# Kernel optimization log

Measured on AMD Instinct MI355X. Metric: run time of the kernel, lower is better.

The kernel has to match this reference:

```python
import jax, jax.numpy as jnp
import numpy as np

NUM_GRAPHS = 256
BN_EPS = 1e-5


def setup_inputs() -> dict:
    key = jax.random.key(0)
    ks = jax.random.split(key, 16)
    N, E, D_IN, D, L = 100000, 1200000, 4, 64, 3
    inp = {
        "x": jax.random.normal(ks[0], (N, D_IN), dtype=jnp.float32),
        "EdgeID": jax.random.randint(ks[1], (2, E), 0, N, dtype=jnp.int64),
        "EdgeAttr": jax.random.uniform(ks[2], (E,), dtype=jnp.float32),
        "batch": jnp.sort(jax.random.randint(ks[3], (N,), 0, NUM_GRAPHS, dtype=jnp.int64)),
        # embedding Linear(4, 64)
        "W_emb": jax.random.normal(ks[4], (D_IN, D), dtype=jnp.float32) * 0.5,
        "b_emb": jax.random.normal(ks[5], (D,), dtype=jnp.float32) * 0.1,
        # LEConv params stacked over layers: lin1 (bias), lin2 (no bias), lin3 (bias)
        "W1": jax.random.normal(ks[6], (L, D, D), dtype=jnp.float32) * 0.125,
        "b1": jax.random.normal(ks[7], (L, D), dtype=jnp.float32) * 0.1,
        "W2": jax.random.normal(ks[8], (L, D, D), dtype=jnp.float32) * 0.125,
        "W3": jax.random.normal(ks[9], (L, D, D), dtype=jnp.float32) * 0.125,
        "b3": jax.random.normal(ks[10], (L, D), dtype=jnp.float32) * 0.1,
        # BatchNorm affine params per layer
        "gamma": jnp.ones((L, D), dtype=jnp.float32),
        "beta": jnp.zeros((L, D), dtype=jnp.float32),
        # MLP head
        "W_l1": jax.random.normal(ks[11], (D, D), dtype=jnp.float32) * 0.125,
        "b_l1": jax.random.normal(ks[12], (D,), dtype=jnp.float32) * 0.1,
        "W_l2": jax.random.normal(ks[13], (D, 3), dtype=jnp.float32) * 0.125,
        "b_l2": jax.random.normal(ks[14], (3,), dtype=jnp.float32) * 0.1,
    }
    return inp


def reference(x, EdgeID, EdgeAttr, batch, W_emb, b_emb, W1, b1, W2, W3, b3,
              gamma, beta, W_l1, b_l1, W_l2, b_l2):
    N = x.shape[0]
    L = W1.shape[0]
    src, dst = EdgeID[0], EdgeID[1]  # message flows src(j) -> dst(i)

    h = x @ W_emb + b_emb  # [N, 64]; F.dropout(training=False) is a no-op
    for i in range(L):
        a = h @ W1[i] + b1[i]               # lin1(x_j)
        b = h @ W2[i]                       # lin2(x_i)
        msg = EdgeAttr[:, None] * (a[src] - b[dst])  # [E, 64]
        agg = jax.ops.segment_sum(msg, dst, num_segments=N)
        h = agg + h @ W3[i] + b3[i]         # LEConv output
        # BatchNorm (training-mode batch stats over nodes)
        mean = jnp.mean(h, axis=0)
        var = jnp.var(h, axis=0)
        h = gamma[i] * (h - mean) * jax.lax.rsqrt(var + BN_EPS) + beta[i]
        h = jax.nn.relu(h)

    # global mean pool over graphs
    ones = jnp.ones((N,), dtype=h.dtype)
    counts = jax.ops.segment_sum(ones, batch, num_segments=NUM_GRAPHS)
    sums = jax.ops.segment_sum(h, batch, num_segments=NUM_GRAPHS)
    g = sums / jnp.maximum(counts, 1.0)[:, None]  # [G, 64]

    pred = jax.nn.relu(g @ W_l1 + b_l1) @ W_l2 + b_l2  # [G, 3]
    return pred
```

## Files before the change

### kernel.cpp

```cpp
#include <hip/hip_runtime.h>

#define BN_EPS 1e-5f

typedef __attribute__((ext_vector_type(8))) short bf16x8;
typedef __attribute__((ext_vector_type(4))) float f32x4;

__global__ void k_hist(const int* __restrict__ dst, int* __restrict__ deg, int E) {
    int e = blockIdx.x * blockDim.x + threadIdx.x;
    if (e < E) atomicAdd(&deg[dst[e]], 1);
}

__global__ __launch_bounds__(256) void k_blocksum(const int* __restrict__ deg,
                                                  int* __restrict__ bsum, int N) {
    __shared__ int red[256];
    int tid = threadIdx.x;
    int base = blockIdx.x * 1024 + tid * 4;
    int s = 0;
    if (base + 3 < N) {
        int4 v = *(const int4*)&deg[base];
        s = v.x + v.y + v.z + v.w;
    } else {
        for (int i = 0; i < 4; ++i) if (base + i < N) s += deg[base + i];
    }
    red[tid] = s;
    __syncthreads();
    for (int d = 128; d > 0; d >>= 1) {
        if (tid < d) red[tid] += red[tid + d];
        __syncthreads();
    }
    if (tid == 0) bsum[blockIdx.x] = red[0];
}

__global__ __launch_bounds__(1024) void k_scanpartials(int* __restrict__ bsum, int nb) {
    __shared__ int t[1024];
    int tid = threadIdx.x;
    int v = (tid < nb) ? bsum[tid] : 0;
    t[tid] = v;
    __syncthreads();
    for (int d = 1; d < 1024; d <<= 1) {
        int u = (tid >= d) ? t[tid - d] : 0;
        __syncthreads();
        t[tid] += u;
        __syncthreads();
    }
    if (tid < nb) bsum[tid] = t[tid] - v;
}

__global__ __launch_bounds__(256) void k_applyscan(const int* __restrict__ deg,
                                                   const int* __restrict__ bsum,
                                                   int* __restrict__ rowptr,
                                                   int* __restrict__ gcur, int N, int E) {
    __shared__ int red[256];
    int tid = threadIdx.x;
    int base = blockIdx.x * 1024 + tid * 4;
    int v0 = 0, v1 = 0, v2 = 0, v3 = 0;
    if (base + 3 < N) {
        int4 v = *(const int4*)&deg[base];
        v0 = v.x; v1 = v.y; v2 = v.z; v3 = v.w;
    } else {
        if (base < N) v0 = deg[base];
        if (base + 1 < N) v1 = deg[base + 1];
        if (base + 2 < N) v2 = deg[base + 2];
        if (base + 3 < N) v3 = deg[base + 3];
    }
    int s = v0 + v1 + v2 + v3;
    red[tid] = s;
    __syncthreads();
    for (int d = 1; d < 256; d <<= 1) {
        int u = (tid >= d) ? red[tid - d] : 0;
        __syncthreads();
        red[tid] += u;
        __syncthreads();
    }
    int off = bsum[blockIdx.x] + red[tid] - s;
    int r0 = off, r1 = off + v0, r2 = r1 + v1, r3 = r2 + v2;
    if (base < N)     rowptr[base] = r0;
    if (base + 1 < N) rowptr[base + 1] = r1;
    if (base + 2 < N) rowptr[base + 2] = r2;
    if (base + 3 < N) rowptr[base + 3] = r3;
    if ((base & 255) == 0 && base < N) gcur[base >> 8] = r0;
    if (blockIdx.x == 0 && tid == 0) rowptr[N] = E;
}

#define ABLK 8192
__global__ __launch_bounds__(1024) void k_binA(const int* __restrict__ src,
                                               const int* __restrict__ dst,
                                               const float* __restrict__ attr,
                                               int* __restrict__ gcur,
                                               unsigned long long* __restrict__ tmp,
                                               int E, int N) {
    __shared__ int hist[1024];
    __shared__ int lcur[1024];
    int tid = threadIdx.x;
    int NB = (N + 255) >> 8;
    int e0 = blockIdx.x * ABLK;
    int e1 = e0 + ABLK; if (e1 > E) e1 = E;
    for (int i = tid; i < NB; i += 1024) hist[i] = 0;
    __syncthreads();
    for (int e = e0 + tid; e < e1; e += 1024) atomicAdd(&hist[dst[e] >> 8], 1);
    __syncthreads();
    for (int b = tid; b < NB; b += 1024) {
        int hc = hist[b];
        lcur[b] = hc ? atomicAdd(&gcur[b], hc) : 0;
    }
    __syncthreads();
    for (int e = e0 + tid; e < e1; e += 1024) {
        int d = dst[e];
        int pos = atomicAdd(&lcur[d >> 8], 1);
        unsigned long long p = ((unsigned long long)__float_as_uint(attr[e]) << 32) |
                               ((unsigned long long)(d & 255) << 24) |
                               (unsigned int)src[e];
        tmp[pos] = p;
    }
}

__global__ __launch_bounds__(256) void k_binB(const int* __restrict__ rowptr,
                                              const unsigned long long* __restrict__ tmp,
                                              unsigned long long* __restrict__ edata,
                                              int N) {
    __shared__ int cur[256];
    int b = blockIdx.x;
    int tid = threadIdx.x;
    int nb0 = b << 8;
    int node = nb0 + tid;
    cur[tid] = (node < N) ? rowptr[node] : 0;
    int beg = rowptr[nb0];
    int endnode = nb0 + 256; if (endnode > N) endnode = N;
    int end = rowptr[endnode];
    __syncthreads();
    for (int e = beg + tid; e < end; e += 256) {
        unsigned long long p = tmp[e];
        int dl = (int)((p >> 24) & 255);
        int pos = atomicAdd(&cur[dl], 1);
        edata[pos] = (p & 0xFFFFFFFF00000000ull) | ((p & 0xFFFFFFull) << 8);
    }
}

__device__ __forceinline__ void bn_coeff(const float* bs, const float* gam,
                                         const float* bet, int c, float inv_n,
                                         float& sc, float& sh) {
    float mean = bs[c] * inv_n;
    float var = bs[64 + c] * inv_n - mean * mean;
    sc = gam[c] * rsqrtf(fmaxf(var, 0.f) + BN_EPS);
    sh = bet[c] - mean * sc;
}

__global__ void k_gather4(const int* __restrict__ rowptr,
                          const unsigned long long* __restrict__ edata,
                          const float* __restrict__ x,
                          float* __restrict__ g4, float* __restrict__ degw, int N) {
    int n = blockIdx.x * blockDim.x + threadIdx.x;
    if (n >= N) return;
    int beg = rowptr[n], end = rowptr[n + 1];
    float4 a0 = {0.f, 0.f, 0.f, 0.f}, a1 = {0.f, 0.f, 0.f, 0.f};
    float wsum = 0.f;
    int e = beg;
    for (; e + 1 < end; e += 2) {
        unsigned long long p0 = edata[e], p1 = edata[e + 1];
        float w0 = __uint_as_float((unsigned)(p0 >> 32));
        float w1 = __uint_as_float((unsigned)(p1 >> 32));
        float4 v0 = *(const float4*)((const char*)x + (((unsigned)p0) >> 4));
        float4 v1 = *(const float4*)((const char*)x + (((unsigned)p1) >> 4));
        a0.x += w0 * v0.x; a0.y += w0 * v0.y; a0.z += w0 * v0.z; a0.w += w0 * v0.w;
        a1.x += w1 * v1.x; a1.y += w1 * v1.y; a1.z += w1 * v1.z; a1.w += w1 * v1.w;
        wsum += w0 + w1;
    }
    if (e < end) {
        unsigned long long p0 = edata[e];
        float w0 = __uint_as_float((unsigned)(p0 >> 32));
        float4 v0 = *(const float4*)((const char*)x + (((unsigned)p0) >> 4));
        a0.x += w0 * v0.x; a0.y += w0 * v0.y; a0.z += w0 * v0.z; a0.w += w0 * v0.w;
        wsum += w0;
    }
    float4 r;
    r.x = a0.x + a1.x; r.y = a0.y + a1.y; r.z = a0.z + a1.z; r.w = a0.w + a1.w;
    *(float4*)&g4[(size_t)n * 4] = r;
    degw[n] = wsum;
}

template <int ACT, int SAVEDW>
__global__ void k_gather(const int* __restrict__ rowptr,
                         const unsigned long long* __restrict__ edata,
                         const float* __restrict__ h,
                         const float* __restrict__ bsp, const float* __restrict__ gamp,
                         const float* __restrict__ betp,
                         float* __restrict__ S, float* __restrict__ degw, int N) {
    int t = blockIdx.x * blockDim.x + threadIdx.x;
    int n = t >> 6, c = t & 63;
    if (n >= N) return;
    unsigned c4 = (unsigned)(c << 2);
    float sc = 1.f, sh = 0.f;
    if (ACT) bn_coeff(bsp, gamp, betp, c, 1.f / (float)N, sc, sh);
    int beg = rowptr[n], end = rowptr[n + 1];
    int len = end - beg;
    float acc[8] = {0.f, 0.f, 0.f, 0.f, 0.f, 0.f, 0.f, 0.f};
    float wsum = 0.f;
    int nFull = len & ~7;
    for (int base = 0; base < nFull; base += 8) {
#pragma unroll
        for (int i = 0; i < 8; ++i) {
            unsigned long long p = edata[beg + base + i];
            float w = __uint_as_float((unsigned)(p >> 32));
            unsigned off = (unsigned)p;
            float v = *(const float*)((const char*)h + (off | c4));
            if (ACT) v = fmaxf(fmaf(v, sc, sh), 0.f);
            acc[i] += w * v;
            if (SAVEDW) wsum += w;
        }
    }
    if (nFull < len) {
#pragma unroll
        for (int i = 0; i < 8; ++i) {
            int idx = nFull + i;
            int ce = beg + (idx < len ? idx : len - 1);
            unsigned long long p = edata[ce];
            float w = (idx < len) ? __uint_as_float((unsigned)(p >> 32)) : 0.f;
            unsigned off = (unsigned)p;
            float v = *(const float*)((const char*)h + (off | c4));
            if (ACT) v = fmaxf(fmaf(v, sc, sh), 0.f);
            acc[i] += w * v;
            if (SAVEDW) wsum += w;
        }
    }
    float r = ((acc[0] + acc[1]) + (acc[2] + acc[3])) +
              ((acc[4] + acc[5]) + (acc[6] + acc[7]));
    S[(size_t)n * 64 + c] = r;
    if (SAVEDW && c == 0) degw[n] = wsum;
}

__device__ __forceinline__ void split_pack8(const float* v, uint4& H, uint4& L) {
    unsigned hb[8], lb[8];
#pragma unroll
    for (int j = 0; j < 8; ++j) {
        unsigned b = __float_as_uint(v[j]);
        unsigned rb = (b + 0x7FFFu + ((b >> 16) & 1u)) & 0xFFFF0000u;
        hb[j] = rb >> 16;
        float lo = v[j] - __uint_as_float(rb);
        lb[j] = __float_as_uint(lo) >> 16;
    }
    H.x = hb[0] | (hb[1] << 16); H.y = hb[2] | (hb[3] << 16);
    H.z = hb[4] | (hb[5] << 16); H.w = hb[6] | (hb[7] << 16);
    L.x = lb[0] | (lb[1] << 16); L.y = lb[2] | (lb[3] << 16);
    L.z = lb[4] | (lb[5] << 16); L.w = lb[6] | (lb[7] << 16);
}

__device__ __forceinline__ void split_frag(const float* w, bf16x8& hi, bf16x8& lo) {
#pragma unroll
    for (int j = 0; j < 8; ++j) {
        unsigned b = __float_as_uint(w[j]);
        unsigned rb = (b + 0x7FFFu + ((b >> 16) & 1u)) & 0xFFFF0000u;
        hi[j] = (short)(rb >> 16);
        float lof = w[j] - __uint_as_float(rb);
        lo[j] = (short)(__float_as_uint(lof) >> 16);
    }
}

template <int ACT, int EMB>
__global__ __launch_bounds__(512) void k_update(
    const float* __restrict__ S, float* __restrict__ h,
    const float* __restrict__ degw,
    const float* __restrict__ xin, const float* __restrict__ g4,
    const float* __restrict__ Wemb, const float* __restrict__ bemb,
    const float* __restrict__ bsp, const float* __restrict__ gamp,
    const float* __restrict__ betp,
    const float* __restrict__ W1, const float* __restrict__ b1,
    const float* __restrict__ W2, const float* __restrict__ W3,
    const float* __restrict__ b3,
    float* __restrict__ bnstats, int N) {
    __shared__ __align__(16) unsigned short sA[16384];
    __shared__ float dwS[64];

    int tid = threadIdx.x;
    int lane = tid & 63;
    int wv = tid >> 6;
    int mg = wv >> 2;
    int nb = wv & 3;
    int c = (nb << 4) | (lane & 15);
    int krow = (lane >> 4) << 3;

    bf16x8 B1h[2], B1l[2], B2h[2], B2l[2], B3h[2], B3l[2];
#pragma unroll
    for (int ks = 0; ks < 2; ++ks) {
        float w1v[8], w2v[8], w3v[8];
        int kb = ks * 32 + krow;
#pragma unroll
        for (int j = 0; j < 8; ++j) {
            int idx = (kb + j) * 64 + c;
            w1v[j] = W1[idx];
            w2v[j] = W2[idx];
            w3v[j] = W3[idx];
        }
        split_frag(w1v, B1h[ks], B1l[ks]);
        split_frag(w2v, B2h[ks], B2l[ks]);
        split_frag(w3v, B3h[ks], B3l[ks]);
    }
    float b1c = b1[c], b3c = b3[c];

    int r = tid >> 3;
    int kg = tid & 7;
    int k0 = kg << 3;
    int slot = ((((r >> 4) * 2 + (kg >> 2)) * 64) + ((kg & 3) << 4) + (r & 15)) * 8;

    float scv[8], shv[8];
    if (ACT) {
        float inv_n = 1.f / (float)N;
#pragma unroll
        for (int j = 0; j < 8; ++j) {
            float mean = bsp[k0 + j] * inv_n;
            float var = bsp[64 + k0 + j] * inv_n - mean * mean;
            float sc = gamp[k0 + j] * rsqrtf(fmaxf(var, 0.f) + BN_EPS);
            scv[j] = sc;
            shv[j] = betp[k0 + j] - mean * sc;
        }
    }
    float we0[8], we1[8], we2[8], we3[8], bev[8];
    if (EMB) {
#pragma unroll
        for (int j = 0; j < 8; ++j) {
            we0[j] = Wemb[k0 + j];
            we1[j] = Wemb[64 + k0 + j];
            we2[j] = Wemb[128 + k0 + j];
            we3[j] = Wemb[192 + k0 + j];
            bev[j] = bemb[k0 + j];
        }
    }

    float bsum = 0.f, bsq = 0.f;
    int numTiles = (N + 63) >> 6;
    for (int tile = blockIdx.x; tile < numTiles; tile += gridDim.x) {
        int n0 = tile << 6;
        __syncthreads();
        {
            int n = n0 + r;
            float sv[8], hv[8];
            if (n < N) {
                if (EMB) {
                    float4 g = *(const float4*)&g4[(size_t)n * 4];
                    float4 xr = *(const float4*)&xin[(size_t)n * 4];
                    float dw = degw[n];
#pragma unroll
                    for (int j = 0; j < 8; ++j) {
                        sv[j] = fmaf(g.x, we0[j], fmaf(g.y, we1[j],
                                 fmaf(g.z, we2[j], fmaf(g.w, we3[j], dw * bev[j]))));
                        hv[j] = fmaf(xr.x, we0[j], fmaf(xr.y, we1[j],
                                 fmaf(xr.z, we2[j], fmaf(xr.w, we3[j], bev[j]))));
                    }
                } else {
                    const float* Sp = &S[(size_t)n * 64 + k0];
                    const float* hp = &h[(size_t)n * 64 + k0];
                    float4 s0_ = *(const float4*)Sp;
                    float4 s1_ = *(const float4*)(Sp + 4);
                    float4 h0_ = *(const float4*)hp;
                    float4 h1_ = *(const float4*)(hp + 4);
                    sv[0]=s0_.x; sv[1]=s0_.y; sv[2]=s0_.z; sv[3]=s0_.w;
                    sv[4]=s1_.x; sv[5]=s1_.y; sv[6]=s1_.z; sv[7]=s1_.w;
                    hv[0]=h0_.x; hv[1]=h0_.y; hv[2]=h0_.z; hv[3]=h0_.w;
                    hv[4]=h1_.x; hv[5]=h1_.y; hv[6]=h1_.z; hv[7]=h1_.w;
                    if (ACT) {
#pragma unroll
                        for (int j = 0; j < 8; ++j)
                            hv[j] = fmaxf(fmaf(hv[j], scv[j], shv[j]), 0.f);
                    }
                }
            } else {
#pragma unroll
                for (int j = 0; j < 8; ++j) { sv[j] = 0.f; hv[j] = 0.f; }
            }
            uint4 H, L;
            split_pack8(sv, H, L);
            *(uint4*)&sA[slot] = H;
            *(uint4*)&sA[4096 + slot] = L;
            split_pack8(hv, H, L);
            *(uint4*)&sA[8192 + slot] = H;
            *(uint4*)&sA[12288 + slot] = L;
            if (tid < 64) dwS[tid] = (n0 + tid < N) ? degw[n0 + tid] : 0.f;
        }
        __syncthreads();
        f32x4 accP[2] = {{0.f,0.f,0.f,0.f},{0.f,0.f,0.f,0.f}};
        f32x4 accN[2] = {{0.f,0.f,0.f,0.f},{0.f,0.f,0.f,0.f}};
#pragma unroll
        for (int ks = 0; ks < 2; ++ks) {
#pragma unroll
            for (int mtg = 0; mtg < 2; ++mtg) {
                int mt = mg * 2 + mtg;
                int base = ((mt * 2 + ks) * 64 + lane) * 8;
                bf16x8 aSh = *(const bf16x8*)&sA[base];
                bf16x8 aSl = *(const bf16x8*)&sA[4096 + base];
                bf16x8 aHh = *(const bf16x8*)&sA[8192 + base];
                bf16x8 aHl = *(const bf16x8*)&sA[12288 + base];
                f32x4 p = accP[mtg], q = accN[mtg];
                p = __builtin_amdgcn_mfma_f32_16x16x32_bf16(aSh, B1h[ks], p, 0, 0, 0);
                p = __builtin_amdgcn_mfma_f32_16x16x32_bf16(aSl, B1h[ks], p, 0, 0, 0);
                p = __builtin_amdgcn_mfma_f32_16x16x32_bf16(aSh, B1l[ks], p, 0, 0, 0);
                p = __builtin_amdgcn_mfma_f32_16x16x32_bf16(aHh, B3h[ks], p, 0, 0, 0);
                p = __builtin_amdgcn_mfma_f32_16x16x32_bf16(aHl, B3h[ks], p, 0, 0, 0);
                p = __builtin_amdgcn_mfma_f32_16x16x32_bf16(aHh, B3l[ks], p, 0, 0, 0);
                q = __builtin_amdgcn_mfma_f32_16x16x32_bf16(aHh, B2h[ks], q, 0, 0, 0);
                q = __builtin_amdgcn_mfma_f32_16x16x32_bf16(aHl, B2h[ks], q, 0, 0, 0);
                q = __builtin_amdgcn_mfma_f32_16x16x32_bf16(aHh, B2l[ks], q, 0, 0, 0);
                accP[mtg] = p; accN[mtg] = q;
            }
        }
#pragma unroll
        for (int mtg = 0; mtg < 2; ++mtg) {
            int rowb = mg * 32 + mtg * 16 + ((lane >> 4) << 2);
            float4 dwv = *(const float4*)&dwS[rowb];
            float dwa[4] = {dwv.x, dwv.y, dwv.z, dwv.w};
#pragma unroll
            for (int j = 0; j < 4; ++j) {
                int n = n0 + rowb + j;
                if (n < N) {
                    float val = accP[mtg][j] - dwa[j] * accN[mtg][j] + dwa[j] * b1c + b3c;
                    h[(size_t)n * 64 + c] = val;
                    bsum += val;
                    bsq += val * val;
                }
            }
        }
    }
    __syncthreads();
    float* red = (float*)sA;
    red[tid] = bsum;
    red[512 + tid] = bsq;
    __syncthreads();
    if (tid < 64) {
        int nb_ = tid >> 4, cl = tid & 15;
        float s = 0.f, qq = 0.f;
#pragma unroll
        for (int i = 0; i < 8; ++i) {
            int t = ((i & 1) << 8) + (nb_ << 6) + ((i >> 1) << 4) + cl;
            s += red[t];
            qq += red[512 + t];
        }
        atomicAdd(&bnstats[tid], s);
        atomicAdd(&bnstats[64 + tid], qq);
    }
}

#define POOL_TILE 128
__global__ __launch_bounds__(256) void k_poolsum(const float* __restrict__ h,
                                                 const int* __restrict__ batch,
                                                 const float* __restrict__ bsp,
                                                 const float* __restrict__ gamp,
                                                 const float* __restrict__ betp,
                                                 float* __restrict__ gsums, int N) {
    int tid = threadIdx.x;
    int c = tid & 63, q = tid >> 6;
    float sc, sh_;
    bn_coeff(bsp, gamp, betp, c, 1.f / (float)N, sc, sh_);
    int n0 = blockIdx.x * POOL_TILE;
    int nEnd = n0 + POOL_TILE; if (nEnd > N) nEnd = N;
    int g = -1;
    float acc = 0.f;
    for (int n = n0 + q; n < nEnd; n += 4) {
        int b = batch[n];
        if (b != g) {
            if (g >= 0) atomicAdd(&gsums[(size_t)g * 64 + c], acc);
            g = b; acc = 0.f;
        }
        acc += fmaxf(fmaf(h[(size_t)n * 64 + c], sc, sh_), 0.f);
    }
    if (g >= 0) atomicAdd(&gsums[(size_t)g * 64 + c], acc);
}

__global__ void k_head(const float* __restrict__ gsums, const int* __restrict__ batch,
                       const float* __restrict__ Wl1, const float* __restrict__ bl1,
                       const float* __restrict__ Wl2, const float* __restrict__ bl2,
                       float* __restrict__ out, int N) {
    int g = blockIdx.x;
    int c = threadIdx.x;
    int lo = 0, hi = N;
    while (lo < hi) { int mid = (lo + hi) >> 1; if (batch[mid] < g) lo = mid + 1; else hi = mid; }
    int start = lo;
    hi = N;
    while (lo < hi) { int mid = (lo + hi) >> 1; if (batch[mid] < g + 1) lo = mid + 1; else hi = mid; }
    int cnt = lo - start;
    float denom = (float)(cnt > 0 ? cnt : 1);
    __shared__ float gS[64], yS[64];
    gS[c] = gsums[(size_t)g * 64 + c] / denom;
    __syncthreads();
    float y = bl1[c];
    for (int k = 0; k < 64; ++k) y += gS[k] * Wl1[k * 64 + c];
    yS[c] = fmaxf(y, 0.f);
    __syncthreads();
    if (c < 3) {
        float o = bl2[c];
        for (int k = 0; k < 64; ++k) o += yS[k] * Wl2[k * 3 + c];
        out[g * 3 + c] = o;
    }
}

extern "C" void kernel_launch(void* const* d_in, const int* in_sizes, int n_in,
                              void* d_out, int out_size, void* d_ws, size_t ws_size,
                              hipStream_t stream) {
    const float* x     = (const float*)d_in[0];
    const int*   eid   = (const int*)d_in[1];
    const float* attr  = (const float*)d_in[2];
    const int*   batch = (const int*)d_in[3];
    const float* Wemb  = (const float*)d_in[4];
    const float* bemb  = (const float*)d_in[5];
    const float* W1    = (const float*)d_in[6];
    const float* b1    = (const float*)d_in[7];
    const float* W2    = (const float*)d_in[8];
    const float* W3    = (const float*)d_in[9];
    const float* b3    = (const float*)d_in[10];
    const float* gamma = (const float*)d_in[11];
    const float* beta  = (const float*)d_in[12];
    const float* Wl1   = (const float*)d_in[13];
    const float* bl1   = (const float*)d_in[14];
    const float* Wl2   = (const float*)d_in[15];
    const float* bl2   = (const float*)d_in[16];

    int N = in_sizes[3];
    int E = in_sizes[2];
    int L = in_sizes[7] / 64;
    int G = out_size / 3;

    const int* src = eid;
    const int* dst = eid + E;

    float* ws      = (float*)d_ws;
    float* h       = ws;
    float* S       = h + (size_t)N * 64;
    float* degw    = S + (size_t)N * 64;
    float* g4      = degw + N;
    float* bnstats = g4 + (size_t)N * 4;
    float* gsums   = bnstats + 3 * 128;
    int*   deg     = (int*)(gsums + (size_t)G * 64);
    int*   rowptr  = deg + N;
    int*   bsum    = rowptr + (N + 2);
    int*   gcur    = bsum + 1024;
    unsigned long long* edata = (unsigned long long*)(gcur + 1024);
    unsigned long long* tmp   = edata + E;

    int nScanBlocks = (N + 1023) / 1024;
    int NB = (N + 255) >> 8;

    hipMemsetAsync(deg, 0, (size_t)N * sizeof(int), stream);
    hipMemsetAsync(bnstats, 0, 3 * 128 * sizeof(float), stream);
    k_hist<<<(E + 255) / 256, 256, 0, stream>>>(dst, deg, E);
    k_blocksum<<<nScanBlocks, 256, 0, stream>>>(deg, bsum, N);
    k_scanpartials<<<1, 1024, 0, stream>>>(bsum, nScanBlocks);
    k_applyscan<<<nScanBlocks, 256, 0, stream>>>(deg, bsum, rowptr, gcur, N, E);
    k_binA<<<(E + ABLK - 1) / ABLK, 1024, 0, stream>>>(src, dst, attr, gcur, tmp, E, N);
    k_binB<<<NB, 256, 0, stream>>>(rowptr, tmp, edata, N);

    int gGrid = (N * 64 + 255) / 256;
    for (int l = 0; l < L; ++l) {
        const float* bsp  = bnstats + (size_t)(l > 0 ? l - 1 : 0) * 128;
        const float* gamp = gamma + (size_t)(l > 0 ? l - 1 : 0) * 64;
        const float* betp = beta + (size_t)(l > 0 ? l - 1 : 0) * 64;
        if (l == 0) {
            k_gather4<<<(N + 255) / 256, 256, 0, stream>>>(rowptr, edata, x, g4, degw, N);
            k_update<0, 1><<<512, 512, 0, stream>>>(S, h, degw, x, g4, Wemb, bemb,
                                                    bsp, gamp, betp,
                                                    W1, b1, W2, W3, b3, bnstats, N);
        } else {
            k_gather<1, 0><<<gGrid, 256, 0, stream>>>(rowptr, edata, h, bsp, gamp, betp,
                                                      S, degw, N);
            k_update<1, 0><<<512, 512, 0, stream>>>(S, h, degw, nullptr, nullptr,
                                                    nullptr, nullptr, bsp, gamp, betp,
                                                    W1 + (size_t)l * 4096, b1 + (size_t)l * 64,
                                                    W2 + (size_t)l * 4096, W3 + (size_t)l * 4096,
                                                    b3 + (size_t)l * 64,
                                                    bnstats + (size_t)l * 128, N);
        }
    }

    hipMemsetAsync(gsums, 0, (size_t)G * 64 * sizeof(float), stream);
    k_poolsum<<<(N + POOL_TILE - 1) / POOL_TILE, 256, 0, stream>>>(
        h, batch, bnstats + (size_t)(L - 1) * 128, gamma + (size_t)(L - 1) * 64,
        beta + (size_t)(L - 1) * 64, gsums, N);
    k_head<<<G, 64, 0, stream>>>(gsums, batch, Wl1, bl1, Wl2, bl2, (float*)d_out, N);
}
```

Baseline: 437.8 us.

## Precompute BN+ReLU activations into fp16 buffer for gather and update

Adds a k_act pass that applies BatchNorm and ReLU once per node and stores the activated features as fp16. The edge gather (k_gather16) and the update kernel then read this half-size buffer instead of the fp32 h, and they no longer recompute the affine and ReLU on every edge read. This halves the bytes moved by the random-access gather, which is the dominant cost. The price is an extra pass over h each layer and fp16 rounding of activations, which may reduce accuracy. The edge encoding now stores the node index rather than a byte offset.

```diff
diff --git a/kernel.cpp b/kernel.cpp
--- a/kernel.cpp
+++ b/kernel.cpp
@@ -132,7 +132,7 @@
         unsigned long long p = tmp[e];
         int dl = (int)((p >> 24) & 255);
         int pos = atomicAdd(&cur[dl], 1);
-        edata[pos] = (p & 0xFFFFFFFF00000000ull) | ((p & 0xFFFFFFull) << 8);
+        edata[pos] = (p & 0xFFFFFFFF00000000ull) | (p & 0xFFFFFFull);
     }
 }
 
@@ -143,6 +143,13 @@
     float var = bs[64 + c] * inv_n - mean * mean;
     sc = gam[c] * rsqrtf(fmaxf(var, 0.f) + BN_EPS);
     sh = bet[c] - mean * sc;
+}
+
+__device__ __forceinline__ float h16lo(unsigned u) {
+    return (float)__builtin_bit_cast(_Float16, (unsigned short)(u & 0xFFFFu));
+}
+__device__ __forceinline__ float h16hi(unsigned u) {
+    return (float)__builtin_bit_cast(_Float16, (unsigned short)(u >> 16));
 }
 
 __global__ void k_gather4(const int* __restrict__ rowptr,
@@ -159,8 +166,8 @@
         unsigned long long p0 = edata[e], p1 = edata[e + 1];
         float w0 = __uint_as_float((unsigned)(p0 >> 32));
         float w1 = __uint_as_float((unsigned)(p1 >> 32));
-        float4 v0 = *(const float4*)((const char*)x + (((unsigned)p0) >> 4));
-        float4 v1 = *(const float4*)((const char*)x + (((unsigned)p1) >> 4));
+        float4 v0 = *(const float4*)((const char*)x + (((unsigned)p0) << 4));
+        float4 v1 = *(const float4*)((const char*)x + (((unsigned)p1) << 4));
         a0.x += w0 * v0.x; a0.y += w0 * v0.y; a0.z += w0 * v0.z; a0.w += w0 * v0.w;
         a1.x += w1 * v1.x; a1.y += w1 * v1.y; a1.z += w1 * v1.z; a1.w += w1 * v1.w;
         wsum += w0 + w1;
@@ -168,7 +175,7 @@
     if (e < end) {
         unsigned long long p0 = edata[e];
         float w0 = __uint_as_float((unsigned)(p0 >> 32));
-        float4 v0 = *(const float4*)((const char*)x + (((unsigned)p0) >> 4));
+        float4 v0 = *(const float4*)((const char*)x + (((unsigned)p0) << 4));
         a0.x += w0 * v0.x; a0.y += w0 * v0.y; a0.z += w0 * v0.z; a0.w += w0 * v0.w;
         wsum += w0;
     }
@@ -178,54 +185,75 @@
     degw[n] = wsum;
 }
 
-template <int ACT, int SAVEDW>
-__global__ void k_gather(const int* __restrict__ rowptr,
-                         const unsigned long long* __restrict__ edata,
-                         const float* __restrict__ h,
-                         const float* __restrict__ bsp, const float* __restrict__ gamp,
-                         const float* __restrict__ betp,
-                         float* __restrict__ S, float* __restrict__ degw, int N) {
+__global__ __launch_bounds__(256) void k_act(const float* __restrict__ h,
+                                             const float* __restrict__ bs,
+                                             const float* __restrict__ gam,
+                                             const float* __restrict__ bet,
+                                             unsigned short* __restrict__ a16,
+                                             int N) {
+    __shared__ float scS[64], shS[64];
+    int tid = threadIdx.x;
+    if (tid < 64) {
+        float sc, sh;
+        bn_coeff(bs, gam, bet, tid, 1.f / (float)N, sc, sh);
+        scS[tid] = sc; shS[tid] = sh;
+    }
+    __syncthreads();
+    int c0 = (tid & 15) << 2;
+    float4 scv = *(const float4*)&scS[c0];
+    float4 shv = *(const float4*)&shS[c0];
+    int total = N << 4;
+    for (int t = blockIdx.x * 256 + tid; t < total; t += gridDim.x * 256) {
+        float4 v = *(const float4*)&h[(size_t)t * 4];
+        float r0 = fmaxf(fmaf(v.x, scv.x, shv.x), 0.f);
+        float r1 = fmaxf(fmaf(v.y, scv.y, shv.y), 0.f);
+        float r2 = fmaxf(fmaf(v.z, scv.z, shv.z), 0.f);
+        float r3 = fmaxf(fmaf(v.w, scv.w, shv.w), 0.f);
+        unsigned q0 = __builtin_bit_cast(unsigned short, (_Float16)r0);
+        unsigned q1 = __builtin_bit_cast(unsigned short, (_Float16)r1);
+        unsigned q2 = __builtin_bit_cast(unsigned short, (_Float16)r2);
+        unsigned q3 = __builtin_bit_cast(unsigned short, (_Float16)r3);
+        uint2 o; o.x = q0 | (q1 << 16); o.y = q2 | (q3 << 16);
+        *(uint2*)&a16[(size_t)t * 4] = o;
+    }
+}
+
+__global__ void k_gather16(const int* __restrict__ rowptr,
+                           const unsigned long long* __restrict__ edata,
+                           const unsigned short* __restrict__ a16,
+                           float* __restrict__ S, int N) {
     int t = blockIdx.x * blockDim.x + threadIdx.x;
     int n = t >> 6, c = t & 63;
     if (n >= N) return;
-    unsigned c4 = (unsigned)(c << 2);
-    float sc = 1.f, sh = 0.f;
-    if (ACT) bn_coeff(bsp, gamp, betp, c, 1.f / (float)N, sc, sh);
+    unsigned c2 = (unsigned)(c << 1);
     int beg = rowptr[n], end = rowptr[n + 1];
     int len = end - beg;
     float acc[8] = {0.f, 0.f, 0.f, 0.f, 0.f, 0.f, 0.f, 0.f};
-    float wsum = 0.f;
     int nFull = len & ~7;
     for (int base = 0; base < nFull; base += 8) {
 #pragma unroll
         for (int i = 0; i < 8; ++i) {
             unsigned long long p = edata[beg + base + i];
             float w = __uint_as_float((unsigned)(p >> 32));
-            unsigned off = (unsigned)p;
-            float v = *(const float*)((const char*)h + (off | c4));
-            if (ACT) v = fmaxf(fmaf(v, sc, sh), 0.f);
-            acc[i] += w * v;
-            if (SAVEDW) wsum += w;
+            unsigned off = ((unsigned)p) << 7;
+            float v = (float)*(const _Float16*)((const char*)a16 + (off | c2));
+            acc[i] = fmaf(w, v, acc[i]);
         }
     }
     if (nFull < len) {
 #pragma unroll
         for (int i = 0; i < 8; ++i) {
             int idx = nFull + i;
-            int ce = beg + (idx < len ? idx : len - 1);
-            unsigned long long p = edata[ce];
+            unsigned long long p = edata[beg + (idx < len ? idx : len - 1)];
             float w = (idx < len) ? __uint_as_float((unsigned)(p >> 32)) : 0.f;
-            unsigned off = (unsigned)p;
-            float v = *(const float*)((const char*)h + (off | c4));
-            if (ACT) v = fmaxf(fmaf(v, sc, sh), 0.f);
-            acc[i] += w * v;
-            if (SAVEDW) wsum += w;
+            unsigned off = ((unsigned)p) << 7;
+            float v = (float)*(const _Float16*)((const char*)a16 + (off | c2));
+            acc[i] = fmaf(w, v, acc[i]);
         }
     }
     float r = ((acc[0] + acc[1]) + (acc[2] + acc[3])) +
               ((acc[4] + acc[5]) + (acc[6] + acc[7]));
     S[(size_t)n * 64 + c] = r;
-    if (SAVEDW && c == 0) degw[n] = wsum;
 }
 
 __device__ __forceinline__ void split_pack8(const float* v, uint4& H, uint4& L) {
@@ -255,14 +283,13 @@
     }
 }
 
-template <int ACT, int EMB>
+template <int PRE, int EMB>
 __global__ __launch_bounds__(512) void k_update(
     const float* __restrict__ S, float* __restrict__ h,
     const float* __restrict__ degw,
     const float* __restrict__ xin, const float* __restrict__ g4,
     const float* __restrict__ Wemb, const float* __restrict__ bemb,
-    const float* __restrict__ bsp, const float* __restrict__ gamp,
-    const float* __restrict__ betp,
+    const unsigned short* __restrict__ a16,
     const float* __restrict__ W1, const float* __restrict__ b1,
     const float* __restrict__ W2, const float* __restrict__ W3,
     const float* __restrict__ b3,
@@ -301,18 +328,6 @@
     int k0 = kg << 3;
     int slot = ((((r >> 4) * 2 + (kg >> 2)) * 64) + ((kg & 3) << 4) + (r & 15)) * 8;
 
-    float scv[8], shv[8];
-    if (ACT) {
-        float inv_n = 1.f / (float)N;
-#pragma unroll
-        for (int j = 0; j < 8; ++j) {
-            float mean = bsp[k0 + j] * inv_n;
-            float var = bsp[64 + k0 + j] * inv_n - mean * mean;
-            float sc = gamp[k0 + j] * rsqrtf(fmaxf(var, 0.f) + BN_EPS);
-            scv[j] = sc;
-            shv[j] = betp[k0 + j] - mean * sc;
-        }
-    }
     float we0[8], we1[8], we2[8], we3[8], bev[8];
     if (EMB) {
 #pragma unroll
@@ -347,20 +362,15 @@
                     }
                 } else {
                     const float* Sp = &S[(size_t)n * 64 + k0];
-                    const float* hp = &h[(size_t)n * 64 + k0];
                     float4 s0_ = *(const float4*)Sp;
                     float4 s1_ = *(const float4*)(Sp + 4);
-                    float4 h0_ = *(const float4*)hp;
-                    float4 h1_ = *(const float4*)(hp + 4);
                     sv[0]=s0_.x; sv[1]=s0_.y; sv[2]=s0_.z; sv[3]=s0_.w;
                     sv[4]=s1_.x; sv[5]=s1_.y; sv[6]=s1_.z; sv[7]=s1_.w;
-                    hv[0]=h0_.x; hv[1]=h0_.y; hv[2]=h0_.z; hv[3]=h0_.w;
-                    hv[4]=h1_.x; hv[5]=h1_.y; hv[6]=h1_.z; hv[7]=h1_.w;
-                    if (ACT) {
-#pragma unroll
-                        for (int j = 0; j < 8; ++j)
-                            hv[j] = fmaxf(fmaf(hv[j], scv[j], shv[j]), 0.f);
-                    }
+                    uint4 hp = *(const uint4*)((const char*)a16 + (((size_t)n) << 7) + (k0 << 1));
+                    hv[0] = h16lo(hp.x); hv[1] = h16hi(hp.x);
+                    hv[2] = h16lo(hp.y); hv[3] = h16hi(hp.y);
+                    hv[4] = h16lo(hp.z); hv[5] = h16hi(hp.z);
+                    hv[6] = h16lo(hp.w); hv[7] = h16hi(hp.w);
                 }
             } else {
 #pragma unroll
@@ -532,6 +542,7 @@
     int*   gcur    = bsum + 1024;
     unsigned long long* edata = (unsigned long long*)(gcur + 1024);
     unsigned long long* tmp   = edata + E;
+    unsigned short* a16 = (unsigned short*)(((uintptr_t)(tmp + E) + 15) & ~(uintptr_t)15);
 
     int nScanBlocks = (N + 1023) / 1024;
     int NB = (N + 255) >> 8;
@@ -547,23 +558,24 @@
 
     int gGrid = (N * 64 + 255) / 256;
     for (int l = 0; l < L; ++l) {
-        const float* bsp  = bnstats + (size_t)(l > 0 ? l - 1 : 0) * 128;
-        const float* gamp = gamma + (size_t)(l > 0 ? l - 1 : 0) * 64;
-        const float* betp = beta + (size_t)(l > 0 ? l - 1 : 0) * 64;
         if (l == 0) {
             k_gather4<<<(N + 255) / 256, 256, 0, stream>>>(rowptr, edata, x, g4, degw, N);
             k_update<0, 1><<<512, 512, 0, stream>>>(S, h, degw, x, g4, Wemb, bemb,
-                                                    bsp, gamp, betp,
+                                                    nullptr,
                                                     W1, b1, W2, W3, b3, bnstats, N);
         } else {
-            k_gather<1, 0><<<gGrid, 256, 0, stream>>>(rowptr, edata, h, bsp, gamp, betp,
-                                                      S, degw, N);
+            k_gather16<<<gGrid, 256, 0, stream>>>(rowptr, edata, a16, S, N);
             k_update<1, 0><<<512, 512, 0, stream>>>(S, h, degw, nullptr, nullptr,
-                                                    nullptr, nullptr, bsp, gamp, betp,
+                                                    nullptr, nullptr, a16,
                                                     W1 + (size_t)l * 4096, b1 + (size_t)l * 64,
                                                     W2 + (size_t)l * 4096, W3 + (size_t)l * 4096,
                                                     b3 + (size_t)l * 64,
                                                     bnstats + (size_t)l * 128, N);
+        }
+        if (l + 1 < L) {
+            k_act<<<1024, 256, 0, stream>>>(h, bnstats + (size_t)l * 128,
+                                            gamma + (size_t)l * 64, beta + (size_t)l * 64,
+                                            a16, N);
         }
     }
 
```

Result: faster. 427.8 us (-2.3%).
